# Performance work log

Hardware: AMD Instinct MI355X
Metric: run time of the kernel (lower is better)

Reference implementation:

```python
import jax, jax.numpy as jnp
import numpy as np

B, S, H = 1, 1024, 2048
NH, NKV, HD = 32, 4, 128
E, K, I = 32, 8, 768
EPS = 1e-06
ROPE_BASE = 1e6


def rmsnorm(x, w, eps=EPS):
    xf = x.astype(jnp.float32)
    var = jnp.mean(xf * xf, axis=-1, keepdims=True)
    return w * (xf * jax.lax.rsqrt(var + eps)).astype(x.dtype)


def apply_rope(x, cos, sin):
    # x: [B,S,N,HD]; cos/sin: [S,HD//2]; interleaved (llama-style) pair rotation
    xr = x.reshape(*x.shape[:-1], HD // 2, 2)
    x0, x1 = xr[..., 0], xr[..., 1]
    c = cos[None, :, None, :]
    s = sin[None, :, None, :]
    o0 = x0 * c - x1 * s
    o1 = x0 * s + x1 * c
    return jnp.stack([o0, o1], axis=-1).reshape(x.shape)


def setup_inputs() -> dict:
    key = jax.random.key(0)
    ks = jax.random.split(key, 16)
    hidden_states = jax.random.normal(ks[0], (B, S, H), dtype=jnp.float32)
    # RoPE angles: positions * inv_freq  -> [S, HD//2]
    inv_freq = 1.0 / (ROPE_BASE ** (np.arange(0, HD, 2, dtype=np.float32) / HD))
    position_embeddings = jnp.asarray(np.arange(S, dtype=np.float32)[:, None] * inv_freq[None, :])
    # causal additive mask [1,1,S,S]
    causal = jnp.tril(jnp.ones((S, S), dtype=bool))
    attention_mask = jnp.where(causal, 0.0, -1e9).astype(jnp.float32)[None, None]
    w = 0.02
    params = {
        'ln1_w': jnp.ones((H,), jnp.float32),
        'ln2_w': jnp.ones((H,), jnp.float32),
        'q_w': w * jax.random.normal(ks[1], (H, NH * HD), jnp.float32),
        'k_w': w * jax.random.normal(ks[2], (H, NKV * HD), jnp.float32),
        'v_w': w * jax.random.normal(ks[3], (H, NKV * HD), jnp.float32),
        'o_w': w * jax.random.normal(ks[4], (NH * HD, H), jnp.float32),
        'qn_w': jnp.ones((HD,), jnp.float32),
        'kn_w': jnp.ones((HD,), jnp.float32),
        'gate_w': w * jax.random.normal(ks[5], (H, E), jnp.float32),
        'wg': w * jax.random.normal(ks[6], (E, H, I), jnp.float32),
        'wu': w * jax.random.normal(ks[7], (E, H, I), jnp.float32),
        'wd': w * jax.random.normal(ks[8], (E, I, H), jnp.float32),
    }
    return {'hidden_states': hidden_states, 'position_embeddings': position_embeddings,
            'attention_mask': attention_mask, 'start_pos': 0, **params}


def reference(hidden_states, position_embeddings, attention_mask, start_pos,
              ln1_w, ln2_w, q_w, k_w, v_w, o_w, qn_w, kn_w, gate_w, wg, wu, wd):
    x = hidden_states  # [B,S,H]
    # --- attention ---
    h = rmsnorm(x, ln1_w)
    q = rmsnorm((h @ q_w).reshape(B, S, NH, HD), qn_w)
    k = rmsnorm((h @ k_w).reshape(B, S, NKV, HD), kn_w)
    v = (h @ v_w).reshape(B, S, NKV, HD)
    cos, sin = jnp.cos(position_embeddings), jnp.sin(position_embeddings)
    q = apply_rope(q, cos, sin)
    k = apply_rope(k, cos, sin)
    q = q.transpose(0, 2, 1, 3)  # [B,NH,S,HD]
    k = jnp.repeat(k.transpose(0, 2, 1, 3), NH // NKV, axis=1)
    v = jnp.repeat(v.transpose(0, 2, 1, 3), NH // NKV, axis=1)
    scores = jnp.einsum('bhqd,bhkd->bhqk', q, k) * (HD ** -0.5) + attention_mask
    attn = jax.nn.softmax(scores, axis=-1)
    o = jnp.einsum('bhqk,bhkd->bhqd', attn, v).transpose(0, 2, 1, 3).reshape(B, S, NH * HD)
    x = x + o @ o_w
    # --- MoE ---
    h = rmsnorm(x, ln2_w).reshape(B * S, H)  # [T,H]
    probs = jax.nn.softmax((h @ gate_w).astype(jnp.float32), axis=-1)
    rw, sel = jax.lax.top_k(probs, K)  # [T,K]
    rw = rw / jnp.sum(rw, axis=-1, keepdims=True)  # norm_topk_prob
    T = B * S
    # dense combine weights [T,E]; zero for unselected experts (same math as loop)
    wte = jnp.zeros((T, E), jnp.float32).at[jnp.arange(T)[:, None], sel].add(rw).astype(h.dtype)
    g = jnp.einsum('th,ehi->tei', h, wg)
    u = jnp.einsum('th,ehi->tei', h, wu)
    act = jax.nn.silu(g) * u  # [T,E,I]
    moe = jnp.einsum('te,tei,eih->th', wte, act, wd)
    return x + moe.reshape(B, S, H)
```

## Files before the change

kernel.cpp:

```cpp
#include <hip/hip_runtime.h>
#include <hip/hip_bf16.h>

#define S_ 1024
#define H_ 2048
#define NH_ 32
#define NKV_ 4
#define HD_ 128
#define NE_ 32
#define TOPK_ 8
#define I_ 768
#define EPS_ 1e-6f
#define QS_ 5120
#define BK2 32
#define NPAR 4

typedef __bf16 bf16_t;
typedef __bf16 bf16x4v __attribute__((ext_vector_type(4)));
typedef __bf16 bf16x8 __attribute__((ext_vector_type(8)));
typedef float f32x4 __attribute__((ext_vector_type(4)));
typedef float f32x16 __attribute__((ext_vector_type(16)));
typedef unsigned short u16_t;
typedef unsigned int uint2v __attribute__((ext_vector_type(2)));
typedef unsigned int uint4v __attribute__((ext_vector_type(4)));

static __device__ __forceinline__ u16_t f2u(float x) {
  return __builtin_bit_cast(u16_t, (__bf16)x);
}
static __device__ __forceinline__ float u2f(u16_t u) {
  return (float)__builtin_bit_cast(__bf16, u);
}

static __device__ __forceinline__ void gload16(const bf16_t* g, bf16_t* l) {
  __builtin_amdgcn_global_load_lds(
      (const __attribute__((address_space(1))) unsigned int*)g,
      (__attribute__((address_space(3))) unsigned int*)l, 16, 0, 0);
}

static __device__ __forceinline__ int tile_lane_off(int lane) {
  return (lane >> 2) * 32 + (((lane & 3) ^ ((lane >> 3) & 3)) << 3);
}

template <bool WF32>
__global__ __launch_bounds__(256) void rmsnorm2_k(const float* __restrict__ x,
                                                  const float* __restrict__ w,
                                                  float* __restrict__ outf,
                                                  bf16_t* __restrict__ outb) {
  int r = blockIdx.x, tid = threadIdx.x;
  const float* xr = x + (size_t)r * H_;
  f32x4 a = *(const f32x4*)(xr + tid * 8);
  f32x4 b = *(const f32x4*)(xr + tid * 8 + 4);
  float ss = 0.f;
#pragma unroll
  for (int i = 0; i < 4; ++i) ss += a[i] * a[i] + b[i] * b[i];
#pragma unroll
  for (int m = 1; m < 64; m <<= 1) ss += __shfl_xor(ss, m);
  __shared__ float wsum[4];
  if ((tid & 63) == 0) wsum[tid >> 6] = ss;
  __syncthreads();
  ss = wsum[0] + wsum[1] + wsum[2] + wsum[3];
  float inv = rsqrtf(ss * (1.0f / H_) + EPS_);
  f32x4 w0 = *(const f32x4*)(w + tid * 8);
  f32x4 w1 = *(const f32x4*)(w + tid * 8 + 4);
  f32x4 o0, o1;
#pragma unroll
  for (int i = 0; i < 4; ++i) { o0[i] = a[i] * inv * w0[i]; o1[i] = b[i] * inv * w1[i]; }
  if constexpr (WF32) {
    *(f32x4*)(outf + (size_t)r * H_ + tid * 8) = o0;
    *(f32x4*)(outf + (size_t)r * H_ + tid * 8 + 4) = o1;
  }
  bf16x8 ob;
#pragma unroll
  for (int i = 0; i < 4; ++i) { ob[i] = (__bf16)o0[i]; ob[i + 4] = (__bf16)o1[i]; }
  *(bf16x8*)(outb + (size_t)r * H_ + tid * 8) = ob;
}

__global__ __launch_bounds__(256) void transp3_k(const float* __restrict__ in,
                                                 bf16_t* __restrict__ out, int R, int C) {
  __shared__ float tile[64][65];
  size_t z = (size_t)blockIdx.z * R * C;
  int tx = threadIdx.x & 15, ty = threadIdx.x >> 4;
  int r0 = blockIdx.y * 64, c0 = blockIdx.x * 64;
#pragma unroll
  for (int i = 0; i < 4; ++i) {
    f32x4 v = *(const f32x4*)(in + z + (size_t)(r0 + ty + i * 16) * C + c0 + tx * 4);
    tile[ty + i * 16][tx * 4 + 0] = v[0];
    tile[ty + i * 16][tx * 4 + 1] = v[1];
    tile[ty + i * 16][tx * 4 + 2] = v[2];
    tile[ty + i * 16][tx * 4 + 3] = v[3];
  }
  __syncthreads();
  int KT = R >> 5;
  int flat = threadIdx.x * 16;
  int lt = flat >> 9;
  int within = flat & 511;
  int nr = within >> 5;
  int kc = within & 31;
  int tn = lt >> 1, tk = lt & 1;
  bf16x8 o0, o1;
#pragma unroll
  for (int j = 0; j < 8; ++j) o0[j] = (bf16_t)tile[tk * 32 + kc + j][tn * 16 + nr];
#pragma unroll
  for (int j = 0; j < 8; ++j) o1[j] = (bf16_t)tile[tk * 32 + kc + 8 + j][tn * 16 + nr];
  size_t tidx = ((size_t)((c0 >> 4) + tn) * KT + (r0 >> 5) + tk) << 9;
  *(bf16x8*)(out + z + tidx + nr * 32 + kc) = o0;
  *(bf16x8*)(out + z + tidx + nr * 32 + kc + 8) = o1;
}

template <int BMT, int BNT, int WM, int WN, typename TC, bool RESID>
__global__ __launch_bounds__(512) void gemmd_k(
    const bf16_t* __restrict__ A, const bf16_t* __restrict__ Bt,
    const float* __restrict__ resid, TC* __restrict__ C, int M, int N, int K) {
  constexpr int MI = BMT / WM / 16;
  constexpr int NI = BNT / WN / 16;
  constexpr int ALW = BMT / 16 / 8;
  constexpr int NBL = BNT / 16;
  static_assert(NBL <= 8, "B wave loads");
  __shared__ __align__(16) bf16_t As[2][BMT][BK2];
  __shared__ __align__(16) bf16_t Bs[2][BNT][BK2];
  int tid = threadIdx.x, lane = tid & 63, w = tid >> 6;
  int m0 = blockIdx.x * BMT, n0 = blockIdx.y * BNT;
  int srow = lane >> 2;
  int schunk = ((lane & 3) ^ ((lane >> 3) & 3)) * 8;
  const bf16_t* asrc[ALW];
#pragma unroll
  for (int i = 0; i < ALW; ++i) {
    int r = (w * ALW + i) * 16 + srow;
    asrc[i] = A + (size_t)(m0 + r) * K + schunk;
  }
  bool hasB = (w < NBL);
  int brow = w * 16;
  const bf16_t* bsrc = nullptr;
  if (hasB)
    bsrc = Bt + ((size_t)((n0 + brow) >> 4) * (K >> 5)) * 512 + tile_lane_off(lane);

  int fr = lane & 15, g = lane >> 4;
  int rk = (g ^ ((fr >> 1) & 3)) * 8;
  int wm = w / WN, wn = w % WN;
  int rbase0 = wm * (BMT / WM), cbase0 = wn * (BNT / WN);
  f32x4 acc[MI][NI] = {};
  int NT = K / BK2;
  {
#pragma unroll
    for (int i = 0; i < ALW; ++i) gload16(asrc[i], &As[0][(w * ALW + i) * 16][0]);
    if (hasB) gload16(bsrc, &Bs[0][brow][0]);
  }
  __syncthreads();
  int cur = 0;
  for (int t = 0; t < NT; ++t) {
    if (t + 1 < NT) {
      int ko = (t + 1) * BK2;
#pragma unroll
      for (int i = 0; i < ALW; ++i) gload16(asrc[i] + ko, &As[cur ^ 1][(w * ALW + i) * 16][0]);
      if (hasB) gload16(bsrc + (size_t)(t + 1) * 512, &Bs[cur ^ 1][brow][0]);
    }
    bf16x8 af[MI], bf[NI];
#pragma unroll
    for (int i = 0; i < MI; ++i) af[i] = *(const bf16x8*)&As[cur][rbase0 + i * 16 + fr][rk];
#pragma unroll
    for (int i = 0; i < NI; ++i) bf[i] = *(const bf16x8*)&Bs[cur][cbase0 + i * 16 + fr][rk];
#pragma unroll
    for (int mi = 0; mi < MI; ++mi)
#pragma unroll
      for (int ni = 0; ni < NI; ++ni)
        acc[mi][ni] = __builtin_amdgcn_mfma_f32_16x16x32_bf16(af[mi], bf[ni], acc[mi][ni], 0, 0, 0);
    __syncthreads();
    cur ^= 1;
  }
  int rbase = g * 4;
#pragma unroll
  for (int mi = 0; mi < MI; ++mi)
#pragma unroll
    for (int ni = 0; ni < NI; ++ni)
#pragma unroll
      for (int r = 0; r < 4; ++r) {
        int gi = m0 + rbase0 + mi * 16 + rbase + r;
        int gc = n0 + cbase0 + ni * 16 + fr;
        float v = acc[mi][ni][r];
        if constexpr (RESID) v += resid[(size_t)gi * N + gc];
        C[(size_t)gi * N + gc] = (TC)v;
      }
}

template <int BMT, int BNT, int WM, int WN, typename TC, bool GATHER, bool SCALE, bool DUAL>
__global__ __launch_bounds__(512) void gemme_k(
    const bf16_t* __restrict__ A, const bf16_t* __restrict__ B1g,
    const bf16_t* __restrict__ B2g, TC* __restrict__ C, bf16_t* __restrict__ act,
    const float* __restrict__ wlist, const int* __restrict__ counts,
    const int* __restrict__ offsets, const int* __restrict__ toklist,
    const int* __restrict__ mslots, const int* __restrict__ meta,
    int* __restrict__ qhead, int NTN, int N, int K) {
  constexpr int MI = BMT / WM / 16;
  constexpr int NI = BNT / WN / 16;
  constexpr int BNTT = BNT * (DUAL ? 2 : 1);
  constexpr int ALW = BMT / 16 / 8;
  constexpr int NBL = BNTT / 16;
  static_assert(NBL <= 8, "B wave loads");
  __shared__ __align__(16) bf16_t As[2][BMT][BK2];
  __shared__ __align__(16) bf16_t Bs[2][BNTT][BK2];
  __shared__ int s_w;
  int tid = threadIdx.x, lane = tid & 63, w = tid >> 6;
  int srow = lane >> 2;
  int schunk = ((lane & 3) ^ ((lane >> 3) & 3)) * 8;
  int tloff = tile_lane_off(lane);
  int fr = lane & 15, g = lane >> 4;
  int rk = (g ^ ((fr >> 1) & 3)) * 8;
  int wm = w / WN, wn = w % WN;
  int rbase0 = wm * (BMT / WM), cbase0 = wn * (BNT / WN);
  int KT = K >> 5;
  int total = meta[0] * NTN;
  for (;;) {
    if (tid == 0) s_w = atomicAdd(qhead, 1);
    __syncthreads();
    int wk = s_w;
    if (wk >= total) return;
    int ms = mslots[wk / NTN];
    int n0 = (wk % NTN) * BNT;
    int e = ms >> 8, m0 = (ms & 255) * BMT;
    int cnt = counts[e], off = offsets[e];
    size_t bs = (size_t)K * N;
    const bf16_t* B1 = B1g + (size_t)e * bs;
    const bf16_t* B2 = DUAL ? (B2g + (size_t)e * bs) : nullptr;
    const bf16_t* asrc[ALW];
#pragma unroll
    for (int i = 0; i < ALW; ++i) {
      int r = (w * ALW + i) * 16 + srow;
      int gr = min(m0 + r, cnt - 1);
      size_t grow;
      if constexpr (GATHER) grow = (size_t)toklist[e * S_ + gr];
      else grow = (size_t)(off + gr);
      asrc[i] = A + grow * (size_t)K + schunk;
    }
    bool hasB = (w < NBL);
    const bf16_t* bsrc = nullptr;
    int brow = w * 16;
    if (hasB) {
      const bf16_t* Bb = (brow < BNT) ? B1 : B2;
      int rr = (brow < BNT) ? brow : brow - BNT;
      bsrc = Bb + ((size_t)((n0 + rr) >> 4) * KT) * 512 + tloff;
    }
    f32x4 acc1[MI][NI] = {};
    f32x4 acc2[DUAL ? MI : 1][DUAL ? NI : 1] = {};
    int NT = K / BK2;
    {
#pragma unroll
      for (int i = 0; i < ALW; ++i) gload16(asrc[i], &As[0][(w * ALW + i) * 16][0]);
      if (hasB) gload16(bsrc, &Bs[0][brow][0]);
    }
    __syncthreads();
    int cur = 0;
    for (int t = 0; t < NT; ++t) {
      if (t + 1 < NT) {
        int ko = (t + 1) * BK2;
#pragma unroll
        for (int i = 0; i < ALW; ++i) gload16(asrc[i] + ko, &As[cur ^ 1][(w * ALW + i) * 16][0]);
        if (hasB) gload16(bsrc + (size_t)(t + 1) * 512, &Bs[cur ^ 1][brow][0]);
      }
      bf16x8 af[MI], b1f[NI], b2f[DUAL ? NI : 1];
#pragma unroll
      for (int i = 0; i < MI; ++i) af[i] = *(const bf16x8*)&As[cur][rbase0 + i * 16 + fr][rk];
#pragma unroll
      for (int i = 0; i < NI; ++i) b1f[i] = *(const bf16x8*)&Bs[cur][cbase0 + i * 16 + fr][rk];
      if constexpr (DUAL) {
#pragma unroll
        for (int i = 0; i < NI; ++i) b2f[i] = *(const bf16x8*)&Bs[cur][BNT + cbase0 + i * 16 + fr][rk];
      }
#pragma unroll
      for (int mi = 0; mi < MI; ++mi)
#pragma unroll
        for (int ni = 0; ni < NI; ++ni) {
          acc1[mi][ni] = __builtin_amdgcn_mfma_f32_16x16x32_bf16(af[mi], b1f[ni], acc1[mi][ni], 0, 0, 0);
          if constexpr (DUAL)
            acc2[mi][ni] = __builtin_amdgcn_mfma_f32_16x16x32_bf16(af[mi], b2f[ni], acc2[mi][ni], 0, 0, 0);
        }
      __syncthreads();
      cur ^= 1;
    }
    int rbase = g * 4;
#pragma unroll
    for (int mi = 0; mi < MI; ++mi)
#pragma unroll
      for (int ni = 0; ni < NI; ++ni)
#pragma unroll
        for (int r = 0; r < 4; ++r) {
          int lr = rbase0 + mi * 16 + rbase + r;
          int gi = m0 + lr;
          if (gi >= cnt) continue;
          int gc = n0 + cbase0 + ni * 16 + fr;
          if constexpr (DUAL) {
            float gv = acc1[mi][ni][r], uv = acc2[mi][ni][r];
            float sig = 1.0f / (1.0f + __expf(-gv));
            act[(size_t)(off + gi) * N + gc] = (bf16_t)(gv * sig * uv);
          } else {
            float v = acc1[mi][ni][r];
            if constexpr (SCALE) v *= wlist[(size_t)e * S_ + gi];
            C[(size_t)(off + gi) * N + gc] = (TC)v;
          }
        }
  }
}

__global__ __launch_bounds__(64) void qkpack_k(const float* __restrict__ qkv,
                                               const float* __restrict__ qn,
                                               const float* __restrict__ kn,
                                               const float* __restrict__ pe,
                                               bf16_t* __restrict__ Q2,
                                               bf16_t* __restrict__ K2) {
  int s = blockIdx.x, hh = blockIdx.y, lane = threadIdx.x;
  const float* ptr;
  const float* w;
  if (hh < NH_) { ptr = qkv + (size_t)s * QS_ + hh * HD_; w = qn; }
  else          { ptr = qkv + (size_t)s * QS_ + NH_ * HD_ + (hh - NH_) * HD_; w = kn; }
  float x0 = ptr[2 * lane], x1 = ptr[2 * lane + 1];
  float ss = x0 * x0 + x1 * x1;
#pragma unroll
  for (int m = 1; m < 64; m <<= 1) ss += __shfl_xor(ss, m);
  float inv = rsqrtf(ss * (1.0f / HD_) + EPS_);
  x0 = x0 * inv * w[2 * lane];
  x1 = x1 * inv * w[2 * lane + 1];
  float ang = pe[(size_t)s * (HD_ / 2) + lane];
  float sn, cs;
  sincosf(ang, &sn, &cs);
  float r0 = x0 * cs - x1 * sn;
  float r1 = x0 * sn + x1 * cs;
  if (hh < NH_) {
    const float scale = 0.08838834764831845f;
    float a = r0 * scale, b = r1 * scale;
    u16_t h0 = f2u(a), h1 = f2u(b);
    unsigned hw = (unsigned)h0 | ((unsigned)h1 << 16);
    unsigned lw = (unsigned)f2u(a - u2f(h0)) | ((unsigned)f2u(b - u2f(h1)) << 16);
    unsigned* base = (unsigned*)(Q2 + ((size_t)s * NH_ + hh) * 256);
    base[lane] = hw;
    base[64 + lane] = lw;
  } else {
    u16_t h0 = f2u(r0), h1 = f2u(r1);
    unsigned hw = (unsigned)h0 | ((unsigned)h1 << 16);
    unsigned lw = (unsigned)f2u(r0 - u2f(h0)) | ((unsigned)f2u(r1 - u2f(h1)) << 16);
    int j = lane >> 2, off = (2 * lane) & 7;
    unsigned* base = (unsigned*)(K2 + ((size_t)(hh - NH_) * S_ + s) * 256);
    base[(((j) ^ (s & 31)) * 8 + off) >> 1] = hw;
    base[(((16 + j) ^ (s & 31)) * 8 + off) >> 1] = lw;
  }
}

__global__ __launch_bounds__(256) void vpack_k(const float* __restrict__ qkv,
                                               bf16_t* __restrict__ V2T) {
  int t = blockIdx.x, kvh = blockIdx.y;
  int kv0 = t * 64;
  bf16_t* dst = V2T + (size_t)(kvh * 16 + t) * 128 * 128;
  const float* vbase = qkv + NH_ * HD_ + NKV_ * HD_ + kvh * HD_;
#pragma unroll
  for (int i = 0; i < 4; ++i) {
    int flat = threadIdx.x + i * 256;
    int kvp = flat >> 5, d4 = (flat & 31) * 4;
    const float* r0 = vbase + (size_t)(kv0 + 2 * kvp) * QS_ + d4;
    const float* r1 = r0 + QS_;
    f32x4 a = *(const f32x4*)r0;
    f32x4 b = *(const f32x4*)r1;
    int kvg = (2 * kvp) >> 3, sub = (2 * kvp) & 7;
#pragma unroll
    for (int e = 0; e < 4; ++e) {
      int d = d4 + e;
      int fsw = (d ^ (d >> 4)) & 15;
      u16_t ha = f2u(a[e]), hb = f2u(b[e]);
      unsigned hw = (unsigned)ha | ((unsigned)hb << 16);
      unsigned lw = (unsigned)f2u(a[e] - u2f(ha)) | ((unsigned)f2u(b[e] - u2f(hb)) << 16);
      unsigned* dd = (unsigned*)(dst + d * 128);
      dd[((kvg ^ fsw) * 8 + sub) >> 1] = hw;
      dd[(((8 + kvg) ^ fsw) * 8 + sub) >> 1] = lw;
    }
  }
}

#define AKV 64
__global__ __launch_bounds__(512, 4) void attn5_k(const bf16_t* __restrict__ Q2,
                                                  const bf16_t* __restrict__ K2,
                                                  const bf16_t* __restrict__ V2T,
                                                  float* __restrict__ Op,
                                                  float* __restrict__ mlp) {
  int q0 = blockIdx.x * 32;
  int kvh = blockIdx.y;
  int par = blockIdx.z;
  int tid = threadIdx.x, lane = tid & 63, w = tid >> 6;
  int g = lane >> 5, c32 = lane & 31;
  int h = kvh * 8 + w;
  int qrow = q0 + c32;
  int last_t = (q0 + 31) >> 6;
  float2* mlv = (float2*)mlp;
  if (par > last_t) {
    if (g == 0) {
      float2 v2; v2.x = -3.0e38f; v2.y = 0.f;
      mlv[((size_t)par * S_ + qrow) * NH_ + h] = v2;
    }
    return;
  }
  __shared__ __align__(16) u16_t Kl[AKV * 256];
  __shared__ __align__(16) u16_t Vl[128 * 128];

  bf16x8 qh[8], ql[8];
  {
    const bf16_t* qp2 = Q2 + ((size_t)qrow * NH_ + h) * 256;
#pragma unroll
    for (int ks = 0; ks < 8; ++ks) {
      qh[ks] = *(const bf16x8*)(qp2 + g * 8 + ks * 16);
      ql[ks] = *(const bf16x8*)(qp2 + 128 + g * 8 + ks * 16);
    }
  }

  f32x16 accO[4] = {};
  float m = -3.0e38f, l = 0.f;

  for (int t = par; t <= last_t; t += NPAR) {
    int kv0 = t * AKV;
    __syncthreads();
    {
      const bf16_t* ksrc = K2 + ((size_t)kvh * S_ + kv0) * 256;
#pragma unroll
      for (int i = 0; i < 4; ++i) {
        int cbase = w * 64 + i * 512;
        gload16(ksrc + (size_t)(cbase + lane) * 8, (bf16_t*)&Kl[cbase * 8]);
      }
    }
    {
      const bf16_t* vsrc = V2T + (size_t)(kvh * 16 + t) * 128 * 128;
#pragma unroll
      for (int i = 0; i < 4; ++i) {
        int cbase = w * 64 + i * 512;
        gload16(vsrc + (size_t)(cbase + lane) * 8, (bf16_t*)&Vl[cbase * 8]);
      }
    }
    __syncthreads();

    f32x16 accS[2] = {};
#pragma unroll
    for (int ks = 0; ks < 8; ++ks) {
      int db = g * 8 + ks * 16;
#pragma unroll
      for (int mf = 0; mf < 2; ++mf) {
        int kvr = c32 + mf * 32;
        bf16x8 ah = *(const bf16x8*)&Kl[kvr * 256 + (((db >> 3)) ^ c32) * 8];
        bf16x8 al = *(const bf16x8*)&Kl[kvr * 256 + ((16 + (db >> 3)) ^ c32) * 8];
        accS[mf] = __builtin_amdgcn_mfma_f32_32x32x16_bf16(ah, qh[ks], accS[mf], 0, 0, 0);
        accS[mf] = __builtin_amdgcn_mfma_f32_32x32x16_bf16(ah, ql[ks], accS[mf], 0, 0, 0);
        accS[mf] = __builtin_amdgcn_mfma_f32_32x32x16_bf16(al, qh[ks], accS[mf], 0, 0, 0);
      }
    }
    float p[2][16];
    float tmax = -3.0e38f;
#pragma unroll
    for (int mf = 0; mf < 2; ++mf)
#pragma unroll
      for (int r = 0; r < 16; ++r) {
        int kvg = kv0 + mf * 32 + (r & 3) + 8 * (r >> 2) + 4 * g;
        float s = (kvg <= qrow) ? accS[mf][r] : -3.0e38f;
        p[mf][r] = s;
        tmax = fmaxf(tmax, s);
      }
    tmax = fmaxf(tmax, __shfl_xor(tmax, 32));
    float mn = fmaxf(m, tmax);
    float sc = __expf(m - mn);
    float ts = 0.f;
#pragma unroll
    for (int mf = 0; mf < 2; ++mf)
#pragma unroll
      for (int r = 0; r < 16; ++r) {
        float e = __expf(p[mf][r] - mn);
        p[mf][r] = e;
        ts += e;
      }
    ts += __shfl_xor(ts, 32);
    l = l * sc + ts;
    m = mn;
#pragma unroll
    for (int r = 0; r < 16; ++r) {
      int row16 = (r & 3) + 8 * (r >> 2) + 4 * g;
      float scr = __shfl(sc, row16);
#pragma unroll
      for (int nf = 0; nf < 4; ++nf) accO[nf][r] *= scr;
    }
#pragma unroll
    for (int ks = 0; ks < 4; ++ks) {
      int k1 = ks & 1, mf = ks >> 1;
      unsigned Lh[4], Ll[4];
#pragma unroll
      for (int i = 0; i < 4; ++i) {
        float a = p[mf][8 * k1 + 2 * i], b = p[mf][8 * k1 + 2 * i + 1];
        u16_t ha = f2u(a), hb = f2u(b);
        Lh[i] = (unsigned)ha | ((unsigned)hb << 16);
        Ll[i] = (unsigned)f2u(a - u2f(ha)) | ((unsigned)f2u(b - u2f(hb)) << 16);
      }
      unsigned Xh[4], Xl[4];
#pragma unroll
      for (int i = 0; i < 4; ++i) {
        Xh[i] = (unsigned)__shfl_xor((int)Lh[i], 32);
        Xl[i] = (unsigned)__shfl_xor((int)Ll[i], 32);
      }
      uint4v fh, fl;
      fh[0] = g ? Xh[2] : Lh[0]; fh[1] = g ? Xh[3] : Lh[1];
      fh[2] = g ? Lh[2] : Xh[0]; fh[3] = g ? Lh[3] : Xh[1];
      fl[0] = g ? Xl[2] : Ll[0]; fl[1] = g ? Xl[3] : Ll[1];
      fl[2] = g ? Ll[2] : Xl[0]; fl[3] = g ? Ll[3] : Xl[1];
      bf16x8 pH = __builtin_bit_cast(bf16x8, fh);
      bf16x8 pL = __builtin_bit_cast(bf16x8, fl);
      int kvb = g * 8 + ks * 16;
#pragma unroll
      for (int nf = 0; nf < 4; ++nf) {
        int d = c32 + nf * 32;
        int fsw = (d ^ (d >> 4)) & 15;
        bf16x8 vh = *(const bf16x8*)&Vl[d * 128 + (((kvb >> 3)) ^ fsw) * 8];
        bf16x8 vl = *(const bf16x8*)&Vl[d * 128 + ((8 + (kvb >> 3)) ^ fsw) * 8];
        accO[nf] = __builtin_amdgcn_mfma_f32_32x32x16_bf16(pH, vh, accO[nf], 0, 0, 0);
        accO[nf] = __builtin_amdgcn_mfma_f32_32x32x16_bf16(pH, vl, accO[nf], 0, 0, 0);
        accO[nf] = __builtin_amdgcn_mfma_f32_32x32x16_bf16(pL, vh, accO[nf], 0, 0, 0);
      }
    }
  }
#pragma unroll
  for (int r = 0; r < 16; ++r) {
    int row16 = (r & 3) + 8 * (r >> 2) + 4 * g;
    int orow = q0 + row16;
#pragma unroll
    for (int nf = 0; nf < 4; ++nf)
      __builtin_nontemporal_store(
          accO[nf][r], &Op[(((size_t)par * S_ + orow) * NH_ + h) * HD_ + nf * 32 + c32]);
  }
  if (g == 0) {
    float2 v2; v2.x = m; v2.y = l;
    mlv[((size_t)par * S_ + qrow) * NH_ + h] = v2;
  }
}

__global__ __launch_bounds__(128) void attnmerge_k(const float* __restrict__ Op,
                                                   const float* __restrict__ mlp,
                                                   bf16_t* __restrict__ o) {
  int row = blockIdx.x, h = blockIdx.y, d = threadIdx.x;
  const float2* mlv = (const float2*)mlp;
  float mm[NPAR], ll[NPAR];
  float M = -3.0e38f;
#pragma unroll
  for (int p = 0; p < NPAR; ++p) {
    float2 v2 = mlv[((size_t)p * S_ + row) * NH_ + h];
    mm[p] = v2.x; ll[p] = v2.y;
    M = fmaxf(M, mm[p]);
  }
  float acc = 0.f, L = 0.f;
#pragma unroll
  for (int p = 0; p < NPAR; ++p) {
    if (ll[p] == 0.f) continue;
    float wp = __expf(mm[p] - M);
    acc += wp * __builtin_nontemporal_load(
                    &Op[(((size_t)p * S_ + row) * NH_ + h) * HD_ + d]);
    L += wp * ll[p];
  }
  o[((size_t)row * NH_ + h) * HD_ + d] = (bf16_t)(acc / L);
}

__global__ __launch_bounds__(256) void router2_k(const float* __restrict__ h2,
                                                 const float* __restrict__ gw,
                                                 int* __restrict__ sel,
                                                 float* __restrict__ wsel) {
  int t = blockIdx.x, tid = threadIdx.x;
  int e = tid & 31, grp = tid >> 5;
  float acc = 0.f;
  for (int kk = grp; kk < H_; kk += 8)
    acc += h2[(size_t)t * H_ + kk] * gw[(size_t)kk * NE_ + e];
  __shared__ float part[8][32];
  part[grp][e] = acc;
  __syncthreads();
  if (tid < 64) {
    int lane = tid;
    float lg = -3.0e38f;
    if (lane < 32) {
      lg = 0.f;
      for (int g = 0; g < 8; ++g) lg += part[g][lane];
    }
    float tm = lg;
#pragma unroll
    for (int mm = 1; mm < 32; mm <<= 1) tm = fmaxf(tm, __shfl_xor(tm, mm));
    if (lane < 32) lg = __expf(lg - tm);
    bool avail = (lane < 32);
    float tot = 0.f;
    int se[TOPK_]; float rw[TOPK_];
#pragma unroll
    for (int kk = 0; kk < TOPK_; ++kk) {
      float val = avail ? lg : -1.f;
      float best = val;
#pragma unroll
      for (int mm = 1; mm < 32; mm <<= 1) best = fmaxf(best, __shfl_xor(best, mm));
      unsigned long long ball = __ballot(avail && (val == best));
      int bi = (int)__builtin_ctzll(ball);
      if (lane == bi) avail = false;
      se[kk] = bi;
      rw[kk] = best;
      tot += best;
    }
    float itot = 1.0f / tot;
    if (lane == 0) {
#pragma unroll
      for (int kk = 0; kk < TOPK_; ++kk) {
        sel[t * TOPK_ + kk] = se[kk];
        wsel[t * TOPK_ + kk] = rw[kk] * itot;
      }
    }
  }
}

__global__ __launch_bounds__(64) void build_k(const int* __restrict__ sel,
                                              const float* __restrict__ wsel,
                                              int* __restrict__ counts,
                                              int* __restrict__ toklist,
                                              float* __restrict__ wlist,
                                              int* __restrict__ pos) {
  int e = blockIdx.x, lane = threadIdx.x;
  int base = 0;
  for (int c = 0; c < S_ / 64; ++c) {
    int t = c * 64 + lane;
    int match = -1;
#pragma unroll
    for (int k = 0; k < TOPK_; ++k)
      if (sel[t * TOPK_ + k] == e) match = k;
    bool flag = (match >= 0);
    unsigned long long mask = __ballot(flag);
    int prefix = __popcll(mask & ((1ull << lane) - 1ull));
    if (flag) {
      int p = base + prefix;
      toklist[e * S_ + p] = t;
      wlist[e * S_ + p] = wsel[t * TOPK_ + match];
      pos[t * TOPK_ + match] = p;
    }
    base += __popcll(mask);
  }
  if (lane == 0) counts[e] = base;
}

__global__ void scan_k(const int* __restrict__ counts, int* __restrict__ offsets,
                       int* __restrict__ mslots, int* __restrict__ meta,
                       int* __restrict__ qheads) {
  if (threadIdx.x == 0 && blockIdx.x == 0) {
    int o = 0, ns = 0;
    for (int e = 0; e < NE_; ++e) {
      offsets[e] = o;
      int c = counts[e];
      for (int m0 = 0; m0 < c; m0 += 128) mslots[ns++] = (e << 8) | (m0 >> 7);
      o += c;
    }
    offsets[NE_] = o;
    meta[0] = ns;
    qheads[0] = 0;
    qheads[1] = 0;
  }
}

__global__ __launch_bounds__(256) void combine_k(const float* __restrict__ x1,
                                                 const bf16_t* __restrict__ pairout,
                                                 const int* __restrict__ sel,
                                                 const int* __restrict__ pos,
                                                 const int* __restrict__ offsets,
                                                 float* __restrict__ out) {
  int t = blockIdx.x, tid = threadIdx.x;
  int slots[TOPK_];
#pragma unroll
  for (int kk = 0; kk < TOPK_; ++kk)
    slots[kk] = offsets[sel[t * TOPK_ + kk]] + pos[t * TOPK_ + kk];
  int c = tid * 8;
  f32x4 s0 = *(const f32x4*)(x1 + (size_t)t * H_ + c);
  f32x4 s1 = *(const f32x4*)(x1 + (size_t)t * H_ + c + 4);
#pragma unroll
  for (int kk = 0; kk < TOPK_; ++kk) {
    bf16x8 pv = *(const bf16x8*)(pairout + (size_t)slots[kk] * H_ + c);
#pragma unroll
    for (int i = 0; i < 4; ++i) { s0[i] += (float)pv[i]; s1[i] += (float)pv[i + 4]; }
  }
  *(f32x4*)(out + (size_t)t * H_ + c) = s0;
  *(f32x4*)(out + (size_t)t * H_ + c + 4) = s1;
}

extern "C" void kernel_launch(void* const* d_in, const int* in_sizes, int n_in,
                              void* d_out, int out_size, void* d_ws, size_t ws_size,
                              hipStream_t stream) {
  const float* hidden = (const float*)d_in[0];
  const float* pe     = (const float*)d_in[1];
  const float* ln1    = (const float*)d_in[4];
  const float* ln2    = (const float*)d_in[5];
  const float* q_w    = (const float*)d_in[6];
  const float* k_w    = (const float*)d_in[7];
  const float* v_w    = (const float*)d_in[8];
  const float* o_w    = (const float*)d_in[9];
  const float* qn     = (const float*)d_in[10];
  const float* kn     = (const float*)d_in[11];
  const float* gate_w = (const float*)d_in[12];
  const float* wg     = (const float*)d_in[13];
  const float* wu     = (const float*)d_in[14];
  const float* wd     = (const float*)d_in[15];
  float* out = (float*)d_out;

  char* p = (char*)d_ws;
  auto alloc = [&](size_t bytes) {
    char* r = p;
    p += (bytes + 255) & ~(size_t)255;
    return r;
  };
  bf16_t* h1b     = (bf16_t*)alloc((size_t)S_ * H_ * 2);
  float*  qkv     = (float*)alloc((size_t)S_ * QS_ * 4);
  bf16_t* Q2      = (bf16_t*)alloc((size_t)S_ * NH_ * 256 * 2);
  bf16_t* K2      = (bf16_t*)alloc((size_t)NKV_ * S_ * 256 * 2);
  bf16_t* V2T     = (bf16_t*)alloc((size_t)NKV_ * 16 * 128 * 128 * 2);
  bf16_t* aob     = (bf16_t*)alloc((size_t)S_ * NH_ * HD_ * 2);
  float*  x1      = (float*)alloc((size_t)S_ * H_ * 4);
  float*  h2      = (float*)alloc((size_t)S_ * H_ * 4);
  bf16_t* h2b     = (bf16_t*)alloc((size_t)S_ * H_ * 2);
  bf16_t* act     = (bf16_t*)alloc((size_t)S_ * TOPK_ * I_ * 2);
  bf16_t* po      = (bf16_t*)alloc((size_t)S_ * TOPK_ * H_ * 2);
  float*  Opart   = (float*)alloc((size_t)NPAR * S_ * NH_ * HD_ * 4);
  float*  mlpart  = (float*)alloc((size_t)NPAR * S_ * NH_ * 8);
  int*    counts  = (int*)alloc(NE_ * 4);
  int*    offs    = (int*)alloc((NE_ + 1) * 4);
  int*    toklist = (int*)alloc((size_t)NE_ * S_ * 4);
  float*  wlist   = (float*)alloc((size_t)NE_ * S_ * 4);
  int*    sel     = (int*)alloc((size_t)S_ * TOPK_ * 4);
  float*  wsel    = (float*)alloc((size_t)S_ * TOPK_ * 4);
  int*    pos     = (int*)alloc((size_t)S_ * TOPK_ * 4);
  int*    mslots  = (int*)alloc(256 * 4);
  int*    meta    = (int*)alloc(4);
  int*    qheads  = (int*)alloc(2 * 4);
  bf16_t* qkvT = (bf16_t*)alloc((size_t)QS_ * H_ * 2);
  bf16_t* owT  = (bf16_t*)alloc((size_t)(NH_ * HD_) * H_ * 2);
  bf16_t* wgT  = (bf16_t*)alloc((size_t)NE_ * H_ * I_ * 2);
  bf16_t* wuT  = (bf16_t*)alloc((size_t)NE_ * H_ * I_ * 2);
  bf16_t* wdT  = (bf16_t*)alloc((size_t)NE_ * I_ * H_ * 2);
  bf16_t* qwTp = qkvT;
  bf16_t* kwTp = qkvT + (size_t)(NH_ * HD_) * H_;
  bf16_t* vwTp = qkvT + (size_t)(NH_ * HD_ + NKV_ * HD_) * H_;

  transp3_k<<<dim3((NH_ * HD_) / 64, H_ / 64, 1), 256, 0, stream>>>(q_w, qwTp, H_, NH_ * HD_);
  transp3_k<<<dim3((NKV_ * HD_) / 64, H_ / 64, 1), 256, 0, stream>>>(k_w, kwTp, H_, NKV_ * HD_);
  transp3_k<<<dim3((NKV_ * HD_) / 64, H_ / 64, 1), 256, 0, stream>>>(v_w, vwTp, H_, NKV_ * HD_);
  transp3_k<<<dim3(H_ / 64, (NH_ * HD_) / 64, 1), 256, 0, stream>>>(o_w, owT, NH_ * HD_, H_);
  transp3_k<<<dim3(I_ / 64, H_ / 64, NE_), 256, 0, stream>>>(wg, wgT, H_, I_);
  transp3_k<<<dim3(I_ / 64, H_ / 64, NE_), 256, 0, stream>>>(wu, wuT, H_, I_);
  transp3_k<<<dim3(H_ / 64, I_ / 64, NE_), 256, 0, stream>>>(wd, wdT, I_, H_);

  rmsnorm2_k<false><<<S_, 256, 0, stream>>>(hidden, ln1, nullptr, h1b);
  gemmd_k<128, 128, 2, 4, float, false>
      <<<dim3(S_ / 128, QS_ / 128), 512, 0, stream>>>(h1b, qkvT, nullptr, qkv, S_, QS_, H_);
  qkpack_k<<<dim3(S_, NH_ + NKV_), 64, 0, stream>>>(qkv, qn, kn, pe, Q2, K2);
  vpack_k<<<dim3(16, NKV_), 256, 0, stream>>>(qkv, V2T);
  attn5_k<<<dim3(S_ / 32, NKV_, NPAR), 512, 0, stream>>>(Q2, K2, V2T, Opart, mlpart);
  attnmerge_k<<<dim3(S_, NH_), 128, 0, stream>>>(Opart, mlpart, aob);
  gemmd_k<128, 128, 2, 4, float, true>
      <<<dim3(S_ / 128, H_ / 128), 512, 0, stream>>>(aob, owT, hidden, x1, S_, H_, NH_ * HD_);
  rmsnorm2_k<true><<<S_, 256, 0, stream>>>(x1, ln2, h2, h2b);
  router2_k<<<S_, 256, 0, stream>>>(h2, gate_w, sel, wsel);
  build_k<<<NE_, 64, 0, stream>>>(sel, wsel, counts, toklist, wlist, pos);
  scan_k<<<1, 64, 0, stream>>>(counts, offs, mslots, meta, qheads);
  gemme_k<128, 64, 4, 2, float, true, false, true>
      <<<1024, 512, 0, stream>>>(h2b, wgT, wuT, nullptr, act, wlist, counts, offs, toklist,
                                 mslots, meta, &qheads[0], I_ / 64, I_, H_);
  gemme_k<128, 128, 2, 4, bf16_t, false, true, false>
      <<<1024, 512, 0, stream>>>(act, wdT, nullptr, po, nullptr, wlist, counts, offs, nullptr,
                                 mslots, meta, &qheads[1], H_ / 128, H_, I_);
  combine_k<<<S_, 256, 0, stream>>>(x1, po, sel, pos, offs, out);
}
```

Measured before the change: 842.8 us.

## Enlarge MoE expert GEMM tiles to 256 rows and balance tile loads across waves

Doubles the row and column tile sizes of both MoE expert GEMMs (gate/up to 256x128 dual, down to 256x256) and changes the expert slot scan to 256-token chunks. The global-to-LDS load is generalized so each wave loads an equal share of the combined A and B 16-row strips, instead of A split across waves and B loaded by a subset. Larger tiles raise arithmetic intensity and cut redundant weight reads per expert, but experts with about 256 tokens yield fewer work items, which risks lower occupancy and more padded rows. The larger LDS footprint and accumulator count per block also increase register pressure.

```diff
diff --git a/kernel.cpp b/kernel.cpp
--- a/kernel.cpp
+++ b/kernel.cpp
@@ -192,9 +192,9 @@
   constexpr int MI = BMT / WM / 16;
   constexpr int NI = BNT / WN / 16;
   constexpr int BNTT = BNT * (DUAL ? 2 : 1);
-  constexpr int ALW = BMT / 16 / 8;
-  constexpr int NBL = BNTT / 16;
-  static_assert(NBL <= 8, "B wave loads");
+  constexpr int TR = BMT / 16 + BNTT / 16;
+  constexpr int TRW = TR / 8;
+  static_assert(TRW * 8 == TR, "tile split");
   __shared__ __align__(16) bf16_t As[2][BMT][BK2];
   __shared__ __align__(16) bf16_t Bs[2][BNTT][BK2];
   __shared__ int s_w;
@@ -220,40 +220,49 @@
     size_t bs = (size_t)K * N;
     const bf16_t* B1 = B1g + (size_t)e * bs;
     const bf16_t* B2 = DUAL ? (B2g + (size_t)e * bs) : nullptr;
-    const bf16_t* asrc[ALW];
-#pragma unroll
-    for (int i = 0; i < ALW; ++i) {
-      int r = (w * ALW + i) * 16 + srow;
-      int gr = min(m0 + r, cnt - 1);
-      size_t grow;
-      if constexpr (GATHER) grow = (size_t)toklist[e * S_ + gr];
-      else grow = (size_t)(off + gr);
-      asrc[i] = A + grow * (size_t)K + schunk;
-    }
-    bool hasB = (w < NBL);
-    const bf16_t* bsrc = nullptr;
-    int brow = w * 16;
-    if (hasB) {
-      const bf16_t* Bb = (brow < BNT) ? B1 : B2;
-      int rr = (brow < BNT) ? brow : brow - BNT;
-      bsrc = Bb + ((size_t)((n0 + rr) >> 4) * KT) * 512 + tloff;
+    const bf16_t* tsrc[TRW];
+    int tstep[TRW], trow[TRW];
+    bool tisA[TRW];
+#pragma unroll
+    for (int i = 0; i < TRW; ++i) {
+      int j = w * TRW + i;
+      if (j < BMT / 16) {
+        int r = j * 16 + srow;
+        int gr = min(m0 + r, cnt - 1);
+        size_t grow;
+        if constexpr (GATHER) grow = (size_t)toklist[e * S_ + gr];
+        else grow = (size_t)(off + gr);
+        tsrc[i] = A + grow * (size_t)K + schunk;
+        tstep[i] = BK2;
+        trow[i] = j * 16;
+        tisA[i] = true;
+      } else {
+        int bt = j - BMT / 16;
+        int rr16 = bt * 16;
+        const bf16_t* Bb = (rr16 < BNT) ? B1 : B2;
+        int rr = (rr16 < BNT) ? rr16 : rr16 - BNT;
+        tsrc[i] = Bb + ((size_t)((n0 + rr) >> 4) * KT) * 512 + tloff;
+        tstep[i] = 512;
+        trow[i] = rr16;
+        tisA[i] = false;
+      }
     }
     f32x4 acc1[MI][NI] = {};
     f32x4 acc2[DUAL ? MI : 1][DUAL ? NI : 1] = {};
     int NT = K / BK2;
     {
 #pragma unroll
-      for (int i = 0; i < ALW; ++i) gload16(asrc[i], &As[0][(w * ALW + i) * 16][0]);
-      if (hasB) gload16(bsrc, &Bs[0][brow][0]);
+      for (int i = 0; i < TRW; ++i)
+        gload16(tsrc[i], tisA[i] ? &As[0][trow[i]][0] : &Bs[0][trow[i]][0]);
     }
     __syncthreads();
     int cur = 0;
     for (int t = 0; t < NT; ++t) {
       if (t + 1 < NT) {
-        int ko = (t + 1) * BK2;
-#pragma unroll
-        for (int i = 0; i < ALW; ++i) gload16(asrc[i] + ko, &As[cur ^ 1][(w * ALW + i) * 16][0]);
-        if (hasB) gload16(bsrc + (size_t)(t + 1) * 512, &Bs[cur ^ 1][brow][0]);
+#pragma unroll
+        for (int i = 0; i < TRW; ++i)
+          gload16(tsrc[i] + (size_t)(t + 1) * tstep[i],
+                  tisA[i] ? &As[cur ^ 1][trow[i]][0] : &Bs[cur ^ 1][trow[i]][0]);
       }
       bf16x8 af[MI], b1f[NI], b2f[DUAL ? NI : 1];
 #pragma unroll
@@ -640,7 +649,7 @@
     for (int e = 0; e < NE_; ++e) {
       offsets[e] = o;
       int c = counts[e];
-      for (int m0 = 0; m0 < c; m0 += 128) mslots[ns++] = (e << 8) | (m0 >> 7);
+      for (int m0 = 0; m0 < c; m0 += 256) mslots[ns++] = (e << 8) | (m0 >> 8);
       o += c;
     }
     offsets[NE_] = o;
@@ -752,11 +761,11 @@
   router2_k<<<S_, 256, 0, stream>>>(h2, gate_w, sel, wsel);
   build_k<<<NE_, 64, 0, stream>>>(sel, wsel, counts, toklist, wlist, pos);
   scan_k<<<1, 64, 0, stream>>>(counts, offs, mslots, meta, qheads);
-  gemme_k<128, 64, 4, 2, float, true, false, true>
-      <<<1024, 512, 0, stream>>>(h2b, wgT, wuT, nullptr, act, wlist, counts, offs, toklist,
-                                 mslots, meta, &qheads[0], I_ / 64, I_, H_);
-  gemme_k<128, 128, 2, 4, bf16_t, false, true, false>
-      <<<1024, 512, 0, stream>>>(act, wdT, nullptr, po, nullptr, wlist, counts, offs, nullptr,
-                                 mslots, meta, &qheads[1], H_ / 128, H_, I_);
+  gemme_k<256, 128, 4, 2, float, true, false, true>
+      <<<512, 512, 0, stream>>>(h2b, wgT, wuT, nullptr, act, wlist, counts, offs, toklist,
+                                mslots, meta, &qheads[0], I_ / 128, I_, H_);
+  gemme_k<256, 256, 2, 4, bf16_t, false, true, false>
+      <<<512, 512, 0, stream>>>(act, wdT, nullptr, po, nullptr, wlist, counts, offs, nullptr,
+                                mslots, meta, &qheads[1], H_ / 256, H_, I_);
   combine_k<<<S_, 256, 0, stream>>>(x1, po, sel, pos, offs, out);
 }
```

Result: slower. 870.6 us (+3.3%).
